# Optimization experiments

Hardware: AMD Instinct MI355X
Metric: run time of the kernel (lower is better)

Reference implementation:

```python
import jax, jax.numpy as jnp
import numpy as np

UNITS = 64

def _tri_indices(u):
    # pairs (a,b) with b>=a in row-major order == tf.boolean_mask(product_mask1)
    pairs = [(a, b) for a in range(u) for b in range(a, u)]
    ia = np.array([p[0] for p in pairs], np.int32)
    ib = np.array([p[1] for p in pairs], np.int32)
    # triples: for product1 index p=(a,b), keep c>=b (derived from mask2 loops)
    ip, ic = [], []
    for p, (a, b) in enumerate(pairs):
        for c in range(b, u):
            ip.append(p)
            ic.append(c)
    return ia, ib, np.array(ip, np.int32), np.array(ic, np.int32)

def setup_inputs() -> dict:
    key = jax.random.key(0)
    k0, k1, k2, k3, k4 = jax.random.split(key, 5)
    B, D, u = 4096, 66, UNITS
    nprod1 = u * (u + 1) // 2            # 2080
    nprod2 = u * (u + 1) * (u + 2) // 6  # 45760
    inputs = jax.random.normal(k0, (B, D), jnp.float32)
    fw1 = jax.random.uniform(k1, (u,), jnp.float32, 0.0, 2.0 * np.pi * 40.0)
    fw2 = jax.random.normal(k2, (u,), jnp.float32) * 0.05
    fb1 = jax.random.normal(k3, (u,), jnp.float32) * 0.05
    wo = jax.random.normal(k4, (u + nprod1 + nprod2, u), jnp.float32) * 0.05
    return {"inputs": inputs, "fw1": fw1, "fw2": fw2, "fb1": fb1, "wo": wo}

def reference(inputs, fw1, fw2, fb1, wo):
    u = fw1.shape[0]
    ia, ib, ip, ic = _tri_indices(u)
    # Fourier features: cos(x * w1 + b1) * w2,  [B, u]
    f = jnp.cos(inputs[:, :u] * fw1 + fb1) * fw2
    # quadratic upper-triangular products, [B, nprod1] (gather instead of dense outer+mask)
    p1 = f[:, ia] * f[:, ib]
    # cubic products c>=b>=a, [B, nprod2]
    p2 = p1[:, ip] * f[:, ic]
    comb = jnp.concatenate([f, p1, p2], axis=1)  # [B, u+nprod1+nprod2]
    pad = jnp.zeros((inputs.shape[0], inputs.shape[1] - u), inputs.dtype)
    return jnp.concatenate([comb @ wo, pad], axis=1) + inputs
```

## Files before the change

### kernel.cpp

```cpp
#include <hip/hip_runtime.h>
#include <hip/hip_bf16.h>

#define NB      4096
#define ND      66
#define NSTEPP  1792
#define KS      64
#define CH      28
#define MB      16
#define FS      72

#define SBLK    NSTEPP
#define FBLK    (NB*FS/256)
#define OBLK    (NB*ND/256)

typedef __attribute__((ext_vector_type(8))) _Float16 f16x8;
typedef __attribute__((ext_vector_type(4))) _Float16 f16x4;
typedef __attribute__((ext_vector_type(4))) float    f32x4;

__device__ __attribute__((aligned(16))) _Float16 g_f[NB * FS];
__device__ __attribute__((aligned(16))) _Float16 g_woTi[(size_t)(NSTEPP + 1) * 2048];
__device__ __attribute__((aligned(16))) _Float16 g_part[(size_t)KS * MB * 4 * 16 * 256];

__constant__ int c_bb[8] = {0, 48, 204, 532, 1096, 1960, 3188, 4844};

__device__ inline unsigned octet_desc(int o) {
    int t = 0;
#pragma unroll
    for (int i = 1; i < 8; ++i) t += (o >= c_bb[i]);
    int li = o - c_bb[t];
    int P = 8 * t + 8, T = P * (P + 1) / 2;
    int s0, s1;
    if (li == 0)       { s0 = 64; s1 = 64; }
    else if (li <= P)  { s0 = li - 1; s1 = 64; }
    else if (li <= P + T) {
        int r = li - P - 1, a = 0;
        while (r >= P - a) { r -= P - a; ++a; }
        s0 = a; s1 = a + r;
    } else             { s0 = 65; s1 = 65; }
    return (unsigned)s0 | ((unsigned)s1 << 8) | ((unsigned)(8 * t) << 16);
}

__global__ void k_prep(const float* __restrict__ inp, const float* __restrict__ fw1,
                       const float* __restrict__ fw2, const float* __restrict__ fb1,
                       const float* __restrict__ wo, float* __restrict__ out) {
    const int bid = blockIdx.x, tid = threadIdx.x;
    if (bid < SBLK) {
        __shared__ unsigned sd[4];
        if (tid < 4) sd[tid] = octet_desc(bid * 4 + tid);
        __syncthreads();
        const int q = tid >> 6, gg = (tid >> 4) & 3, rl = tid & 15;
        const unsigned d = sd[gg];
        const int s0 = d & 255, s1 = (d >> 8) & 255, cb = d >> 16;
        const int n = q * 16 + rl;
        f16x8 v;
        if (s0 == 64) {
#pragma unroll
            for (int j = 0; j < 8; ++j) v[j] = (_Float16)wo[(cb + j) * 64 + n];
        } else if (s0 < 64 && s1 == 64) {
            int base = 64 + s0 * (129 - s0) / 2 + (cb - s0);
#pragma unroll
            for (int j = 0; j < 8; ++j)
                v[j] = (cb + j >= s0) ? (_Float16)wo[(base + j) * 64 + n] : (_Float16)0.f;
        } else if (s0 < 64) {
            int a = s0, b = s1;
            int TP = 45760 - (64 - a) * (65 - a) * (66 - a) / 6;
            int RB = b * (129 - b) / 2 - a * (129 - a) / 2;
            int base = 2144 + TP + RB + (cb - b);
#pragma unroll
            for (int j = 0; j < 8; ++j)
                v[j] = (cb + j >= b) ? (_Float16)wo[(base + j) * 64 + n] : (_Float16)0.f;
        } else {
#pragma unroll
            for (int j = 0; j < 8; ++j) v[j] = (_Float16)0.f;
        }
        *(f16x8*)(g_woTi + (size_t)bid * 2048 + tid * 8) = v;
    } else if (bid < SBLK + FBLK) {
        int i = (bid - SBLK) * 256 + tid;
        int r = i / FS, c = i - r * FS;
        float v;
        if (c < 64)       v = cosf(inp[r * ND + c] * fw1[c] + fb1[c]) * fw2[c];
        else if (c == 64) v = 1.0f;
        else              v = 0.0f;
        g_f[i] = (_Float16)v;
    } else {
        int i = (bid - SBLK - FBLK) * 256 + tid;
        out[i] = inp[i];
    }
}

__global__ __launch_bounds__(256, 4) void k_gemm() {
    __shared__ __attribute__((aligned(16))) _Float16 fl[256 * FS];
    __shared__ __attribute__((aligned(16))) unsigned ldescT[4 * 32];
    const int mb = blockIdx.x, ks = blockIdx.y, tid = threadIdx.x;
    const int s0c = ks * CH;

    {
        const uint4* src = (const uint4*)(g_f + (size_t)mb * 256 * FS);
        uint4* dst = (uint4*)fl;
        for (int e = tid; e < 256 * FS * 2 / 16; e += 256) dst[e] = src[e];
        if (tid < 128) {
            int gg = tid >> 5, s = tid & 31;
            ldescT[tid] = (s < CH) ? octet_desc((s0c + s) * 4 + gg) : (65u | (65u << 8));
        }
    }
    __syncthreads();

    const int wave = tid >> 6, lane = tid & 63, rl = lane & 15, g = lane >> 4;
    const _Float16* fr0 = fl + (wave * 64 +  0 + rl) * FS;
    const _Float16* fr1 = fl + (wave * 64 + 16 + rl) * FS;
    const _Float16* fr2 = fl + (wave * 64 + 32 + rl) * FS;
    const _Float16* fr3 = fl + (wave * 64 + 48 + rl) * FS;

    f32x4 acc[4][4];
#pragma unroll
    for (int a = 0; a < 4; ++a)
#pragma unroll
        for (int q = 0; q < 4; ++q) acc[a][q] = f32x4{0.f, 0.f, 0.f, 0.f};

    f16x8 c0{}, c1{}, c2{}, c3{};
    _Float16 fa0 = 0, fa1 = 0, fa2 = 0, fa3 = 0;
    int cbPrev = -1, siPrev = -1;

    const _Float16* bptr = g_woTi + (size_t)s0c * 2048 + lane * 8;
    f16x8 B0 = *(const f16x8*)(bptr +    0);
    f16x8 B1 = *(const f16x8*)(bptr +  512);
    f16x8 B2 = *(const f16x8*)(bptr + 1024);
    f16x8 B3 = *(const f16x8*)(bptr + 1536);
    bptr += 2048;

#define STEP(dv)                                                               \
    {                                                                          \
        const int si0 = (dv) & 255, si1 = ((dv) >> 8) & 255;                   \
        const int cb = __builtin_amdgcn_readfirstlane((dv) >> 16);             \
        if (__any(si0 != siPrev)) {                                            \
            siPrev = si0;                                                      \
            fa0 = fr0[si0]; fa1 = fr1[si0]; fa2 = fr2[si0]; fa3 = fr3[si0];    \
        }                                                                      \
        if (cb != cbPrev) {                                                    \
            cbPrev = cb;                                                       \
            c0 = *(const f16x8*)(fr0 + cb); c1 = *(const f16x8*)(fr1 + cb);    \
            c2 = *(const f16x8*)(fr2 + cb); c3 = *(const f16x8*)(fr3 + cb);    \
        }                                                                      \
        f16x8 nB0 = *(const f16x8*)(bptr +    0);                              \
        f16x8 nB1 = *(const f16x8*)(bptr +  512);                              \
        f16x8 nB2 = *(const f16x8*)(bptr + 1024);                              \
        f16x8 nB3 = *(const f16x8*)(bptr + 1536);                              \
        bptr += 2048;                                                          \
        const _Float16 p0 = fa0 * fr0[si1], p1 = fa1 * fr1[si1];               \
        const _Float16 p2 = fa2 * fr2[si1], p3 = fa3 * fr3[si1];               \
        const f16x8 a0 = c0 * p0, a1 = c1 * p1, a2 = c2 * p2, a3 = c3 * p3;    \
        acc[0][0] = __builtin_amdgcn_mfma_f32_16x16x32_f16(a0, B0, acc[0][0], 0, 0, 0); \
        acc[0][1] = __builtin_amdgcn_mfma_f32_16x16x32_f16(a0, B1, acc[0][1], 0, 0, 0); \
        acc[0][2] = __builtin_amdgcn_mfma_f32_16x16x32_f16(a0, B2, acc[0][2], 0, 0, 0); \
        acc[0][3] = __builtin_amdgcn_mfma_f32_16x16x32_f16(a0, B3, acc[0][3], 0, 0, 0); \
        acc[1][0] = __builtin_amdgcn_mfma_f32_16x16x32_f16(a1, B0, acc[1][0], 0, 0, 0); \
        acc[1][1] = __builtin_amdgcn_mfma_f32_16x16x32_f16(a1, B1, acc[1][1], 0, 0, 0); \
        acc[1][2] = __builtin_amdgcn_mfma_f32_16x16x32_f16(a1, B2, acc[1][2], 0, 0, 0); \
        acc[1][3] = __builtin_amdgcn_mfma_f32_16x16x32_f16(a1, B3, acc[1][3], 0, 0, 0); \
        acc[2][0] = __builtin_amdgcn_mfma_f32_16x16x32_f16(a2, B0, acc[2][0], 0, 0, 0); \
        acc[2][1] = __builtin_amdgcn_mfma_f32_16x16x32_f16(a2, B1, acc[2][1], 0, 0, 0); \
        acc[2][2] = __builtin_amdgcn_mfma_f32_16x16x32_f16(a2, B2, acc[2][2], 0, 0, 0); \
        acc[2][3] = __builtin_amdgcn_mfma_f32_16x16x32_f16(a2, B3, acc[2][3], 0, 0, 0); \
        acc[3][0] = __builtin_amdgcn_mfma_f32_16x16x32_f16(a3, B0, acc[3][0], 0, 0, 0); \
        acc[3][1] = __builtin_amdgcn_mfma_f32_16x16x32_f16(a3, B1, acc[3][1], 0, 0, 0); \
        acc[3][2] = __builtin_amdgcn_mfma_f32_16x16x32_f16(a3, B2, acc[3][2], 0, 0, 0); \
        acc[3][3] = __builtin_amdgcn_mfma_f32_16x16x32_f16(a3, B3, acc[3][3], 0, 0, 0); \
        B0 = nB0; B1 = nB1; B2 = nB2; B3 = nB3;                                \
    }

    const unsigned* dT = ldescT + g * 32;
    for (int s2 = 0; s2 < CH; s2 += 2) {
        uint2 dd = *(const uint2*)(dT + s2);
        STEP(dd.x);
        STEP(dd.y);
    }
#undef STEP

    _Float16* pp = g_part + ((((size_t)ks * MB + mb) * 4 + wave) * 16) * 256;
#pragma unroll
    for (int a = 0; a < 4; ++a)
#pragma unroll
        for (int q = 0; q < 4; ++q) {
            f16x4 v;
            v[0] = (_Float16)acc[a][q][0]; v[1] = (_Float16)acc[a][q][1];
            v[2] = (_Float16)acc[a][q][2]; v[3] = (_Float16)acc[a][q][3];
            *(f16x4*)(pp + (a * 4 + q) * 256 + lane * 4) = v;
        }
}

__global__ void k_reduce(const float* __restrict__ inp, float* __restrict__ out) {
    int t = blockIdx.x * 256 + threadIdx.x;
    int c = t & 63, rg = t >> 6;
    int mb = rg >> 6, wave = (rg >> 4) & 3, a = (rg >> 2) & 3, g = rg & 3;
    int q = c >> 4, rl = c & 15, lane = g * 16 + rl;
    int rbase = mb * 256 + wave * 64 + a * 16 + g * 4;
    float acc[4];
#pragma unroll
    for (int i2 = 0; i2 < 4; ++i2) acc[i2] = inp[(rbase + i2) * ND + c];
    const _Float16* pp = g_part + ((((size_t)mb * 4 + wave) * 16) + a * 4 + q) * 256 + lane * 4;
#pragma unroll
    for (int ks = 0; ks < KS; ++ks) {
        const f16x4 p = *(const f16x4*)(pp + (size_t)ks * MB * 4 * 16 * 256);
#pragma unroll
        for (int i2 = 0; i2 < 4; ++i2) acc[i2] += (float)p[i2];
    }
#pragma unroll
    for (int i2 = 0; i2 < 4; ++i2) out[(rbase + i2) * ND + c] = acc[i2];
}

extern "C" void kernel_launch(void* const* d_in, const int* in_sizes, int n_in,
                              void* d_out, int out_size, void* d_ws, size_t ws_size,
                              hipStream_t stream) {
    const float* inp = (const float*)d_in[0];
    const float* fw1 = (const float*)d_in[1];
    const float* fw2 = (const float*)d_in[2];
    const float* fb1 = (const float*)d_in[3];
    const float* wo  = (const float*)d_in[4];
    float* out = (float*)d_out;

    k_prep<<<SBLK + FBLK + OBLK, 256, 0, stream>>>(inp, fw1, fw2, fb1, wo, out);
    k_gemm<<<dim3(MB, KS), 256, 0, stream>>>();
    k_reduce<<<256, 256, 0, stream>>>(inp, out);
}
```

Measured before the change: 48.85 us.

## Drop operand-reuse branches in GEMM step, unroll by four, shrink output copy

The GEMM inner step no longer caches the A-side factors behind wave-uniform branches. It reloads the si0/si1 scalars and the c-block vectors from LDS on every step, which removes divergence checks and loop-carried state so the compiler can schedule the loads freely. The loop now handles four descriptor steps per iteration with unroll 1 and a uint4 descriptor load. The prep kernel copies only the two padding columns of the input to the output instead of the full matrix, since k_reduce writes the first 64 columns. In exchange there is more LDS traffic per step.

```diff
diff --git a/kernel.cpp b/kernel.cpp
--- a/kernel.cpp
+++ b/kernel.cpp
@@ -11,7 +11,7 @@
 
 #define SBLK    NSTEPP
 #define FBLK    (NB*FS/256)
-#define OBLK    (NB*ND/256)
+#define PBLK    32
 
 typedef __attribute__((ext_vector_type(8))) _Float16 f16x8;
 typedef __attribute__((ext_vector_type(4))) _Float16 f16x4;
@@ -84,7 +84,8 @@
         g_f[i] = (_Float16)v;
     } else {
         int i = (bid - SBLK - FBLK) * 256 + tid;
-        out[i] = inp[i];
+        int r = i >> 1, c = 64 + (i & 1);
+        out[r * ND + c] = inp[r * ND + c];
     }
 }
 
@@ -117,10 +118,6 @@
 #pragma unroll
         for (int q = 0; q < 4; ++q) acc[a][q] = f32x4{0.f, 0.f, 0.f, 0.f};
 
-    f16x8 c0{}, c1{}, c2{}, c3{};
-    _Float16 fa0 = 0, fa1 = 0, fa2 = 0, fa3 = 0;
-    int cbPrev = -1, siPrev = -1;
-
     const _Float16* bptr = g_woTi + (size_t)s0c * 2048 + lane * 8;
     f16x8 B0 = *(const f16x8*)(bptr +    0);
     f16x8 B1 = *(const f16x8*)(bptr +  512);
@@ -131,24 +128,19 @@
 #define STEP(dv)                                                               \
     {                                                                          \
         const int si0 = (dv) & 255, si1 = ((dv) >> 8) & 255;                   \
-        const int cb = __builtin_amdgcn_readfirstlane((dv) >> 16);             \
-        if (__any(si0 != siPrev)) {                                            \
-            siPrev = si0;                                                      \
-            fa0 = fr0[si0]; fa1 = fr1[si0]; fa2 = fr2[si0]; fa3 = fr3[si0];    \
-        }                                                                      \
-        if (cb != cbPrev) {                                                    \
-            cbPrev = cb;                                                       \
-            c0 = *(const f16x8*)(fr0 + cb); c1 = *(const f16x8*)(fr1 + cb);    \
-            c2 = *(const f16x8*)(fr2 + cb); c3 = *(const f16x8*)(fr3 + cb);    \
-        }                                                                      \
+        const int cb  = ((dv) >> 16) & 255;                                    \
         f16x8 nB0 = *(const f16x8*)(bptr +    0);                              \
         f16x8 nB1 = *(const f16x8*)(bptr +  512);                              \
         f16x8 nB2 = *(const f16x8*)(bptr + 1024);                              \
         f16x8 nB3 = *(const f16x8*)(bptr + 1536);                              \
         bptr += 2048;                                                          \
-        const _Float16 p0 = fa0 * fr0[si1], p1 = fa1 * fr1[si1];               \
-        const _Float16 p2 = fa2 * fr2[si1], p3 = fa3 * fr3[si1];               \
-        const f16x8 a0 = c0 * p0, a1 = c1 * p1, a2 = c2 * p2, a3 = c3 * p3;    \
+        const _Float16 p0 = fr0[si0] * fr0[si1], p1 = fr1[si0] * fr1[si1];     \
+        const _Float16 p2 = fr2[si0] * fr2[si1], p3 = fr3[si0] * fr3[si1];     \
+        const f16x8 c0v = *(const f16x8*)(fr0 + cb);                           \
+        const f16x8 c1v = *(const f16x8*)(fr1 + cb);                           \
+        const f16x8 c2v = *(const f16x8*)(fr2 + cb);                           \
+        const f16x8 c3v = *(const f16x8*)(fr3 + cb);                           \
+        const f16x8 a0 = c0v * p0, a1 = c1v * p1, a2 = c2v * p2, a3 = c3v * p3;\
         acc[0][0] = __builtin_amdgcn_mfma_f32_16x16x32_f16(a0, B0, acc[0][0], 0, 0, 0); \
         acc[0][1] = __builtin_amdgcn_mfma_f32_16x16x32_f16(a0, B1, acc[0][1], 0, 0, 0); \
         acc[0][2] = __builtin_amdgcn_mfma_f32_16x16x32_f16(a0, B2, acc[0][2], 0, 0, 0); \
@@ -169,10 +161,13 @@
     }
 
     const unsigned* dT = ldescT + g * 32;
-    for (int s2 = 0; s2 < CH; s2 += 2) {
-        uint2 dd = *(const uint2*)(dT + s2);
+#pragma unroll 1
+    for (int s4 = 0; s4 < CH; s4 += 4) {
+        uint4 dd = *(const uint4*)(dT + s4);
         STEP(dd.x);
         STEP(dd.y);
+        STEP(dd.z);
+        STEP(dd.w);
     }
 #undef STEP
 
@@ -218,7 +213,7 @@
     const float* wo  = (const float*)d_in[4];
     float* out = (float*)d_out;
 
-    k_prep<<<SBLK + FBLK + OBLK, 256, 0, stream>>>(inp, fw1, fw2, fb1, wo, out);
+    k_prep<<<SBLK + FBLK + PBLK, 256, 0, stream>>>(inp, fw1, fw2, fb1, wo, out);
     k_gemm<<<dim3(MB, KS), 256, 0, stream>>>();
     k_reduce<<<256, 256, 0, stream>>>(inp, out);
 }
```

Result: slower. 75.26 us (+54.1%).

## Use two waves per GEMM block with 128 rows each; copy only pad columns

Applied to the files above, without the earlier changes.

The GEMM block drops from four waves to two, and each wave now covers 128 rows (8 row tiles) instead of 64. Each loaded B fragment therefore feeds twice as many MFMAs, which halves global B traffic per row. The cost is a much larger accumulator set (128 fp32 registers) and lower wave parallelism per block, so register pressure or spills and weaker latency hiding are risks. The prep kernel also stops copying the whole input into the output and writes only the two pad columns, since the reduce kernel already writes columns 0-63.

```diff
diff --git a/kernel.cpp b/kernel.cpp
--- a/kernel.cpp
+++ b/kernel.cpp
@@ -11,7 +11,7 @@
 
 #define SBLK    NSTEPP
 #define FBLK    (NB*FS/256)
-#define OBLK    (NB*ND/256)
+#define PBLK    32
 
 typedef __attribute__((ext_vector_type(8))) _Float16 f16x8;
 typedef __attribute__((ext_vector_type(4))) _Float16 f16x4;
@@ -19,7 +19,7 @@
 
 __device__ __attribute__((aligned(16))) _Float16 g_f[NB * FS];
 __device__ __attribute__((aligned(16))) _Float16 g_woTi[(size_t)(NSTEPP + 1) * 2048];
-__device__ __attribute__((aligned(16))) _Float16 g_part[(size_t)KS * MB * 4 * 16 * 256];
+__device__ __attribute__((aligned(16))) _Float16 g_part[(size_t)KS * MB * 16384];
 
 __constant__ int c_bb[8] = {0, 48, 204, 532, 1096, 1960, 3188, 4844};
 
@@ -84,11 +84,12 @@
         g_f[i] = (_Float16)v;
     } else {
         int i = (bid - SBLK - FBLK) * 256 + tid;
-        out[i] = inp[i];
-    }
-}
-
-__global__ __launch_bounds__(256, 4) void k_gemm() {
+        int r = i >> 1, c = 64 + (i & 1);
+        out[r * ND + c] = inp[r * ND + c];
+    }
+}
+
+__global__ __launch_bounds__(128, 2) void k_gemm() {
     __shared__ __attribute__((aligned(16))) _Float16 fl[256 * FS];
     __shared__ __attribute__((aligned(16))) unsigned ldescT[4 * 32];
     const int mb = blockIdx.x, ks = blockIdx.y, tid = threadIdx.x;
@@ -97,8 +98,8 @@
     {
         const uint4* src = (const uint4*)(g_f + (size_t)mb * 256 * FS);
         uint4* dst = (uint4*)fl;
-        for (int e = tid; e < 256 * FS * 2 / 16; e += 256) dst[e] = src[e];
-        if (tid < 128) {
+        for (int e = tid; e < 256 * FS * 2 / 16; e += 128) dst[e] = src[e];
+        {
             int gg = tid >> 5, s = tid & 31;
             ldescT[tid] = (s < CH) ? octet_desc((s0c + s) * 4 + gg) : (65u | (65u << 8));
         }
@@ -106,19 +107,18 @@
     __syncthreads();
 
     const int wave = tid >> 6, lane = tid & 63, rl = lane & 15, g = lane >> 4;
-    const _Float16* fr0 = fl + (wave * 64 +  0 + rl) * FS;
-    const _Float16* fr1 = fl + (wave * 64 + 16 + rl) * FS;
-    const _Float16* fr2 = fl + (wave * 64 + 32 + rl) * FS;
-    const _Float16* fr3 = fl + (wave * 64 + 48 + rl) * FS;
-
-    f32x4 acc[4][4];
-#pragma unroll
-    for (int a = 0; a < 4; ++a)
+    const _Float16* frb = fl + (wave * 128 + rl) * FS;
+
+    f32x4 acc[8][4];
+#pragma unroll
+    for (int a = 0; a < 8; ++a)
 #pragma unroll
         for (int q = 0; q < 4; ++q) acc[a][q] = f32x4{0.f, 0.f, 0.f, 0.f};
 
-    f16x8 c0{}, c1{}, c2{}, c3{};
-    _Float16 fa0 = 0, fa1 = 0, fa2 = 0, fa3 = 0;
+    f16x8 cv[8];
+    _Float16 fa[8];
+#pragma unroll
+    for (int a = 0; a < 8; ++a) { cv[a] = f16x8{}; fa[a] = (_Float16)0.f; }
     int cbPrev = -1, siPrev = -1;
 
     const _Float16* bptr = g_woTi + (size_t)s0c * 2048 + lane * 8;
@@ -134,41 +134,34 @@
         const int cb = __builtin_amdgcn_readfirstlane((dv) >> 16);             \
         if (__any(si0 != siPrev)) {                                            \
             siPrev = si0;                                                      \
-            fa0 = fr0[si0]; fa1 = fr1[si0]; fa2 = fr2[si0]; fa3 = fr3[si0];    \
+            _Pragma("unroll")                                                  \
+            for (int a = 0; a < 8; ++a) fa[a] = frb[a * 16 * FS + si0];        \
         }                                                                      \
         if (cb != cbPrev) {                                                    \
             cbPrev = cb;                                                       \
-            c0 = *(const f16x8*)(fr0 + cb); c1 = *(const f16x8*)(fr1 + cb);    \
-            c2 = *(const f16x8*)(fr2 + cb); c3 = *(const f16x8*)(fr3 + cb);    \
+            _Pragma("unroll")                                                  \
+            for (int a = 0; a < 8; ++a)                                        \
+                cv[a] = *(const f16x8*)(frb + a * 16 * FS + cb);               \
         }                                                                      \
         f16x8 nB0 = *(const f16x8*)(bptr +    0);                              \
         f16x8 nB1 = *(const f16x8*)(bptr +  512);                              \
         f16x8 nB2 = *(const f16x8*)(bptr + 1024);                              \
         f16x8 nB3 = *(const f16x8*)(bptr + 1536);                              \
         bptr += 2048;                                                          \
-        const _Float16 p0 = fa0 * fr0[si1], p1 = fa1 * fr1[si1];               \
-        const _Float16 p2 = fa2 * fr2[si1], p3 = fa3 * fr3[si1];               \
-        const f16x8 a0 = c0 * p0, a1 = c1 * p1, a2 = c2 * p2, a3 = c3 * p3;    \
-        acc[0][0] = __builtin_amdgcn_mfma_f32_16x16x32_f16(a0, B0, acc[0][0], 0, 0, 0); \
-        acc[0][1] = __builtin_amdgcn_mfma_f32_16x16x32_f16(a0, B1, acc[0][1], 0, 0, 0); \
-        acc[0][2] = __builtin_amdgcn_mfma_f32_16x16x32_f16(a0, B2, acc[0][2], 0, 0, 0); \
-        acc[0][3] = __builtin_amdgcn_mfma_f32_16x16x32_f16(a0, B3, acc[0][3], 0, 0, 0); \
-        acc[1][0] = __builtin_amdgcn_mfma_f32_16x16x32_f16(a1, B0, acc[1][0], 0, 0, 0); \
-        acc[1][1] = __builtin_amdgcn_mfma_f32_16x16x32_f16(a1, B1, acc[1][1], 0, 0, 0); \
-        acc[1][2] = __builtin_amdgcn_mfma_f32_16x16x32_f16(a1, B2, acc[1][2], 0, 0, 0); \
-        acc[1][3] = __builtin_amdgcn_mfma_f32_16x16x32_f16(a1, B3, acc[1][3], 0, 0, 0); \
-        acc[2][0] = __builtin_amdgcn_mfma_f32_16x16x32_f16(a2, B0, acc[2][0], 0, 0, 0); \
-        acc[2][1] = __builtin_amdgcn_mfma_f32_16x16x32_f16(a2, B1, acc[2][1], 0, 0, 0); \
-        acc[2][2] = __builtin_amdgcn_mfma_f32_16x16x32_f16(a2, B2, acc[2][2], 0, 0, 0); \
-        acc[2][3] = __builtin_amdgcn_mfma_f32_16x16x32_f16(a2, B3, acc[2][3], 0, 0, 0); \
-        acc[3][0] = __builtin_amdgcn_mfma_f32_16x16x32_f16(a3, B0, acc[3][0], 0, 0, 0); \
-        acc[3][1] = __builtin_amdgcn_mfma_f32_16x16x32_f16(a3, B1, acc[3][1], 0, 0, 0); \
-        acc[3][2] = __builtin_amdgcn_mfma_f32_16x16x32_f16(a3, B2, acc[3][2], 0, 0, 0); \
-        acc[3][3] = __builtin_amdgcn_mfma_f32_16x16x32_f16(a3, B3, acc[3][3], 0, 0, 0); \
+        _Pragma("unroll")                                                      \
+        for (int a = 0; a < 8; ++a) {                                          \
+            const _Float16 p = fa[a] * frb[a * 16 * FS + si1];                 \
+            const f16x8 av = cv[a] * p;                                        \
+            acc[a][0] = __builtin_amdgcn_mfma_f32_16x16x32_f16(av, B0, acc[a][0], 0, 0, 0); \
+            acc[a][1] = __builtin_amdgcn_mfma_f32_16x16x32_f16(av, B1, acc[a][1], 0, 0, 0); \
+            acc[a][2] = __builtin_amdgcn_mfma_f32_16x16x32_f16(av, B2, acc[a][2], 0, 0, 0); \
+            acc[a][3] = __builtin_amdgcn_mfma_f32_16x16x32_f16(av, B3, acc[a][3], 0, 0, 0); \
+        }                                                                      \
         B0 = nB0; B1 = nB1; B2 = nB2; B3 = nB3;                                \
     }
 
     const unsigned* dT = ldescT + g * 32;
+#pragma unroll 1
     for (int s2 = 0; s2 < CH; s2 += 2) {
         uint2 dd = *(const uint2*)(dT + s2);
         STEP(dd.x);
@@ -176,9 +169,9 @@
     }
 #undef STEP
 
-    _Float16* pp = g_part + ((((size_t)ks * MB + mb) * 4 + wave) * 16) * 256;
-#pragma unroll
-    for (int a = 0; a < 4; ++a)
+    _Float16* pp = g_part + ((size_t)ks * MB + mb) * 16384 + wave * 8192;
+#pragma unroll
+    for (int a = 0; a < 8; ++a)
 #pragma unroll
         for (int q = 0; q < 4; ++q) {
             f16x4 v;
@@ -191,16 +184,17 @@
 __global__ void k_reduce(const float* __restrict__ inp, float* __restrict__ out) {
     int t = blockIdx.x * 256 + threadIdx.x;
     int c = t & 63, rg = t >> 6;
-    int mb = rg >> 6, wave = (rg >> 4) & 3, a = (rg >> 2) & 3, g = rg & 3;
+    int mb = rg >> 6, wave = (rg >> 5) & 1, a = (rg >> 2) & 7, g = rg & 3;
     int q = c >> 4, rl = c & 15, lane = g * 16 + rl;
-    int rbase = mb * 256 + wave * 64 + a * 16 + g * 4;
+    int rbase = mb * 256 + wave * 128 + a * 16 + g * 4;
     float acc[4];
 #pragma unroll
     for (int i2 = 0; i2 < 4; ++i2) acc[i2] = inp[(rbase + i2) * ND + c];
-    const _Float16* pp = g_part + ((((size_t)mb * 4 + wave) * 16) + a * 4 + q) * 256 + lane * 4;
+    const _Float16* pp = g_part + (size_t)mb * 16384 + wave * 8192
+                       + (a * 4 + q) * 256 + lane * 4;
 #pragma unroll
     for (int ks = 0; ks < KS; ++ks) {
-        const f16x4 p = *(const f16x4*)(pp + (size_t)ks * MB * 4 * 16 * 256);
+        const f16x4 p = *(const f16x4*)(pp + (size_t)ks * MB * 16384);
 #pragma unroll
         for (int i2 = 0; i2 < 4; ++i2) acc[i2] += (float)p[i2];
     }
@@ -218,7 +212,7 @@
     const float* wo  = (const float*)d_in[4];
     float* out = (float*)d_out;
 
-    k_prep<<<SBLK + FBLK + OBLK, 256, 0, stream>>>(inp, fw1, fw2, fb1, wo, out);
-    k_gemm<<<dim3(MB, KS), 256, 0, stream>>>();
+    k_prep<<<SBLK + FBLK + PBLK, 256, 0, stream>>>(inp, fw1, fw2, fb1, wo, out);
+    k_gemm<<<dim3(MB, KS), 128, 0, stream>>>();
     k_reduce<<<256, 256, 0, stream>>>(inp, out);
 }
```

Result: slower. 50.16 us (+2.7%).
